# Kernel tuning notes

Measured on AMD Instinct MI355X. Metric: run time of the kernel, lower is better.

The kernel has to match this reference:

```python
import jax, jax.numpy as jnp
import numpy as np

N = 100000
E = 1250000
D = 64
K = 3
A_COEF = 1.0
B_COEF = 1.0
L_DOM = -1.0
R_DOM = 1.0


def setup_inputs() -> dict:
    key = jax.random.key(0)
    k1, k2, k3, k4, k5 = jax.random.split(key, 5)
    x = jax.random.normal(k1, (N, D), dtype=jnp.float32)
    edge_index = jax.random.randint(k2, (2, E), 0, N, dtype=jnp.int64)
    edge_weight = jax.random.uniform(k3, (E,), dtype=jnp.float32)
    alpha_params = jnp.ones((K + 1,), dtype=jnp.float32)
    lin_w = jax.random.normal(k4, ((K + 1) * D, D), dtype=jnp.float32) / np.sqrt((K + 1) * D)
    lin_b = jnp.zeros((D,), dtype=jnp.float32)
    return {"x": x, "edge_index": edge_index, "edge_weight": edge_weight,
            "alpha_params": alpha_params, "lin_w": lin_w, "lin_b": lin_b}


def reference(x, edge_index, edge_weight, alpha_params, lin_w, lin_b):
    row, col = edge_index[0], edge_index[1]
    # gcn normalization: deg from source nodes, deg<0.5 -> +1
    deg = jax.ops.segment_sum(jnp.ones((E,), x.dtype), row, num_segments=N)
    deg = jnp.where(deg < 0.5, deg + 1.0, deg)
    dis = deg ** -0.5
    val = dis[row] * edge_weight * dis[col]  # [E]

    def spmm(h):  # adj @ h : out[row] += val * h[col]
        return jax.ops.segment_sum(val[:, None] * h[col], row, num_segments=N)

    alphas = jnp.tanh(alpha_params)  # basealpha = 1.0
    a, b, l, r = A_COEF, B_COEF, L_DOM, R_DOM
    xs = [x]
    for L in range(1, K + 1):
        Ax = spmm(xs[-1])
        if L == 1:
            coef1 = (a - b) / 2 - (a + b + 2) / 2 * ((l + r) / (r - l))
            coef2 = (a + b + 2) / (r - l)
            nxt = alphas[0] * (coef1 * xs[-1] + coef2 * Ax)
        else:
            coef_l = 2 * L * (L + a + b) * (2 * L - 2 + a + b)
            coef_lm1_1 = (2 * L + a + b - 1) * (2 * L + a + b) * (2 * L + a + b - 2)
            coef_lm1_2 = (2 * L + a + b - 1) * (a ** 2 - b ** 2)
            coef_lm2 = 2 * (L - 1 + a) * (L - 1 + b) * (2 * L + a + b)
            tmp1 = alphas[L - 1] * (coef_lm1_1 / coef_l)
            tmp2 = alphas[L - 1] * (coef_lm1_2 / coef_l)
            tmp3 = alphas[L - 1] * alphas[L - 2] * (coef_lm2 / coef_l)
            tmp1_2 = tmp1 * (2.0 / (r - l))
            tmp2_2 = tmp1 * ((r + l) / (r - l)) + tmp2
            nxt = tmp1_2 * Ax - tmp2_2 * xs[-1] - tmp3 * xs[-2]
        xs.append(nxt)
    x_cat = jnp.concatenate(xs, axis=1)  # [N, (K+1)*D]
    return x_cat @ lin_w + lin_b
```

## Files before the change

### kernel.cpp

```cpp
#include <hip/hip_runtime.h>
#include <hip/hip_bf16.h>
#include <math.h>

#define NN 100000
#define EE 1250000
#define DD 64

typedef __attribute__((ext_vector_type(8))) short short8;
typedef __attribute__((ext_vector_type(4))) float f32x4;

__device__ __forceinline__ unsigned short f2b(float f) {
    unsigned u = __float_as_uint(f);
    u += 0x7fffu + ((u >> 16) & 1u);
    return (unsigned short)(u >> 16);
}
__device__ __forceinline__ float b2f(unsigned short h) {
    return __uint_as_float(((unsigned)h) << 16);
}

__global__ __launch_bounds__(256) void scan_a(const int* __restrict__ degi,
                                              int* __restrict__ rowStart,
                                              int* __restrict__ bs, int N) {
    __shared__ int s[256];
    int tid = threadIdx.x;
    int i = blockIdx.x * 256 + tid;
    int v = (i < N) ? degi[i] : 0;
    s[tid] = v;
    __syncthreads();
    for (int off = 1; off < 256; off <<= 1) {
        int t = (tid >= off) ? s[tid - off] : 0;
        __syncthreads();
        s[tid] += t;
        __syncthreads();
    }
    if (i < N) rowStart[i] = s[tid] - v;
    if (tid == 255) bs[blockIdx.x] = s[255];
}

__global__ __launch_bounds__(512) void scan_b(int* __restrict__ bs, int nb) {
    __shared__ int s[512];
    int tid = threadIdx.x;
    int v = (tid < nb) ? bs[tid] : 0;
    s[tid] = v;
    __syncthreads();
    for (int off = 1; off < 512; off <<= 1) {
        int t = (tid >= off) ? s[tid - off] : 0;
        __syncthreads();
        s[tid] += t;
        __syncthreads();
    }
    if (tid < nb) bs[tid] = s[tid] - v;
}

__global__ __launch_bounds__(256) void scan_c(int* __restrict__ rowStart,
                                              const int* __restrict__ bs,
                                              int N, int E) {
    int i = blockIdx.x * 256 + threadIdx.x;
    if (i < N) rowStart[i] += bs[blockIdx.x];
    if (i == 0) rowStart[N] = E;
}

__global__ __launch_bounds__(256) void dis_kernel(const int* __restrict__ degi,
                                                  float* __restrict__ dis, int N) {
    int i = blockIdx.x * 256 + threadIdx.x;
    if (i >= N) return;
    int d = degi[i];
    float df = (d == 0) ? 1.0f : (float)d;
    dis[i] = 1.0f / sqrtf(df);
}

#define NSL 125
#define SLR 800
#define NSEG 16
#define SEGCAP 768
#define CPAD 16
#define VSCL (1.0f / 32768.0f)
__global__ __launch_bounds__(256) void binA(const int* __restrict__ row,
                                            const int* __restrict__ col,
                                            const float* __restrict__ w,
                                            uint2* __restrict__ sbuf,
                                            int* __restrict__ segCnt, int E4) {
    __shared__ int cnt[NSL];
    __shared__ int base[NSL];
    int tid = threadIdx.x;
    if (tid < NSL) cnt[tid] = 0;
    __syncthreads();
    int g = blockIdx.x & (NSEG - 1);
    int i4 = blockIdx.x * 256 + tid;
    bool act = (i4 < E4);
    int4 r4, c4;
    float4 w4;
    int sl[4], loc[4], rk[4];
    unsigned evp[4];
    if (act) {
        r4 = ((const int4*)row)[i4];
        c4 = ((const int4*)col)[i4];
        w4 = ((const float4*)w)[i4];
        int rr[4] = {r4.x, r4.y, r4.z, r4.w};
        int cc[4] = {c4.x, c4.y, c4.z, c4.w};
        float ww[4] = {w4.x, w4.y, w4.z, w4.w};
        #pragma unroll
        for (int k = 0; k < 4; ++k) {
            int r = rr[k], c = cc[k];
            int wq = (int)(ww[k] * 32768.0f + 0.5f);
            wq = (wq > 32767) ? 32767 : wq;
            evp[k] = ((unsigned)c << 15) | (unsigned)wq;
            rk[k] = r;
            sl[k] = r / SLR;
            loc[k] = atomicAdd(&cnt[sl[k]], 1);
        }
    }
    __syncthreads();
    if (tid < NSL) {
        int c = cnt[tid];
        if (c) base[tid] = atomicAdd(&segCnt[(tid * NSEG + g) * CPAD], c);
    }
    __syncthreads();
    if (act) {
        #pragma unroll
        for (int k = 0; k < 4; ++k) {
            int p = base[sl[k]] + loc[k];
            if (p < SEGCAP)
                sbuf[(size_t)(sl[k] * NSEG + g) * SEGCAP + p] =
                    make_uint2(evp[k], (unsigned)rk[k]);
        }
    }
}

__global__ __launch_bounds__(512) void deg_slice(const uint2* __restrict__ sbuf,
                                                 const int* __restrict__ segCnt,
                                                 int* __restrict__ degi) {
    __shared__ int dcnt[SLR];
    __shared__ int scnt[NSEG];
    int tid = threadIdx.x;
    int s = blockIdx.x;
    int r0 = s * SLR;
    for (int i = tid; i < SLR; i += 512) dcnt[i] = 0;
    if (tid < NSEG) {
        int c = segCnt[(s * NSEG + tid) * CPAD];
        scnt[tid] = (c > SEGCAP) ? SEGCAP : c;
    }
    __syncthreads();
    for (int slot = tid * 4; slot < NSEG * SEGCAP; slot += 2048) {
        int g = slot / SEGCAP;
        int off = slot - g * SEGCAP;
        int cg = scnt[g];
        if (off >= cg) continue;
        const uint2* seg = sbuf + (size_t)(s * NSEG + g) * SEGCAP;
        uint4 a = *(const uint4*)(seg + off);
        uint4 b = *(const uint4*)(seg + off + 2);
        atomicAdd(&dcnt[(int)a.y - r0], 1);
        if (off + 1 < cg) atomicAdd(&dcnt[(int)a.w - r0], 1);
        if (off + 2 < cg) atomicAdd(&dcnt[(int)b.y - r0], 1);
        if (off + 3 < cg) atomicAdd(&dcnt[(int)b.w - r0], 1);
    }
    __syncthreads();
    for (int i = tid; i < SLR; i += 512) {
        int gr = r0 + i;
        if (gr < NN) degi[gr] = dcnt[i];
    }
}

__global__ __launch_bounds__(512) void binB(const uint2* __restrict__ sbuf,
                                            const int* __restrict__ segCnt,
                                            const int* __restrict__ rowStart,
                                            const float* __restrict__ dis,
                                            unsigned* __restrict__ ev) {
    __shared__ int curs[SLR];
    __shared__ int rs[SLR];
    __shared__ float dsl[SLR];
    __shared__ int scnt[NSEG];
    int tid = threadIdx.x;
    int s = blockIdx.x;
    int r0 = s * SLR;
    for (int i = tid; i < SLR; i += 512) {
        curs[i] = 0;
        int gr = r0 + i;
        rs[i] = (gr < NN) ? rowStart[gr] : 0;
        dsl[i] = (gr < NN) ? dis[gr] : 1.0f;
    }
    if (tid < NSEG) {
        int c = segCnt[(s * NSEG + tid) * CPAD];
        scnt[tid] = (c > SEGCAP) ? SEGCAP : c;
    }
    __syncthreads();
    for (int slot = tid * 4; slot < NSEG * SEGCAP; slot += 2048) {
        int g = slot / SEGCAP;
        int off = slot - g * SEGCAP;
        int cg = scnt[g];
        if (off >= cg) continue;
        const uint2* seg = sbuf + (size_t)(s * NSEG + g) * SEGCAP;
        uint4 a = *(const uint4*)(seg + off);
        uint4 b = *(const uint4*)(seg + off + 2);
        unsigned pk[4] = {a.x, a.z, b.x, b.z};
        unsigned rr[4] = {a.y, a.w, b.y, b.w};
        int nv = cg - off;
        nv = (nv > 4) ? 4 : nv;
        #pragma unroll 4
        for (int k = 0; k < 4; ++k) {
            if (k >= nv) break;
            int rl = (int)rr[k] - r0;
            int c = (int)(pk[k] >> 15);
            float wv = (float)(pk[k] & 0x7fffu) * VSCL;
            float v = dsl[rl] * wv * dis[c];
            int vq = (int)(v * 32768.0f + 0.5f);
            vq = (vq > 32767) ? 32767 : vq;
            ev[rs[rl] + atomicAdd(&curs[rl], 1)] = ((unsigned)c << 15) | (unsigned)vq;
        }
    }
}

__global__ void coef_kernel(const float* __restrict__ ap, float* __restrict__ coef) {
    if (threadIdx.x != 0 || blockIdx.x != 0) return;
    const float a = 1.0f, b = 1.0f, l = -1.0f, r = 1.0f;
    float als[3];
    als[0] = tanhf(ap[0]);
    als[1] = tanhf(ap[1]);
    als[2] = tanhf(ap[2]);
    float coef1 = (a - b) * 0.5f - (a + b + 2.0f) * 0.5f * ((l + r) / (r - l));
    float coef2 = (a + b + 2.0f) / (r - l);
    coef[0] = als[0] * coef1;
    coef[1] = als[0] * coef2;
    for (int L = 2; L <= 3; ++L) {
        float Lf = (float)L;
        float coef_l     = 2.0f * Lf * (Lf + a + b) * (2.0f * Lf - 2.0f + a + b);
        float coef_lm1_1 = (2.0f * Lf + a + b - 1.0f) * (2.0f * Lf + a + b) * (2.0f * Lf + a + b - 2.0f);
        float coef_lm1_2 = (2.0f * Lf + a + b - 1.0f) * (a * a - b * b);
        float coef_lm2   = 2.0f * (Lf - 1.0f + a) * (Lf - 1.0f + b) * (2.0f * Lf + a + b);
        float tmp1   = als[L - 1] * (coef_lm1_1 / coef_l);
        float tmp2   = als[L - 1] * (coef_lm1_2 / coef_l);
        float tmp3   = als[L - 1] * als[L - 2] * (coef_lm2 / coef_l);
        float tmp1_2 = tmp1 * (2.0f / (r - l));
        float tmp2_2 = tmp1 * ((r + l) / (r - l)) + tmp2;
        int base = 2 + (L - 2) * 3;
        coef[base + 0] = tmp1_2;
        coef[base + 1] = tmp2_2;
        coef[base + 2] = tmp3;
    }
}

__global__ __launch_bounds__(256) void tobf16(const float4* __restrict__ in,
                                              ushort4* __restrict__ outb, int n4) {
    int i = blockIdx.x * 256 + threadIdx.x;
    if (i >= n4) return;
    float4 v = in[i];
    ushort4 o;
    o.x = f2b(v.x); o.y = f2b(v.y); o.z = f2b(v.z); o.w = f2b(v.w);
    outb[i] = o;
}

__global__ __launch_bounds__(256) void wt_kernel(const float* __restrict__ W,
                                                 unsigned short* __restrict__ Wt) {
    int idx = blockIdx.x * 256 + threadIdx.x;
    int n = idx >> 8, k = idx & 255;
    Wt[idx] = f2b(W[k * 64 + n]);
}

template <int MODE>
__global__ __launch_bounds__(256) void spmm_fused(const int* __restrict__ rowStart,
                                                  const unsigned* __restrict__ ev,
                                                  const ushort4* __restrict__ hb,
                                                  const ushort4* __restrict__ xm1,
                                                  const ushort4* __restrict__ xm2,
                                                  ushort4* __restrict__ outb,
                                                  const float* __restrict__ coef,
                                                  int cbase, int N) {
    int t = blockIdx.x * 256 + threadIdx.x;
    int r = t >> 4;
    if (r >= N) return;
    int q = t & 15;
    int s0 = rowStart[r];
    int s1 = rowStart[r + 1];
    float4 acc = make_float4(0.f, 0.f, 0.f, 0.f);
    int j = s0;
    for (; j + 3 < s1; j += 4) {
        unsigned u0 = ev[j];
        unsigned u1 = ev[j + 1];
        unsigned u2 = ev[j + 2];
        unsigned u3 = ev[j + 3];
        ushort4 h0 = hb[(size_t)(u0 >> 15) * 16 + q];
        ushort4 h1 = hb[(size_t)(u1 >> 15) * 16 + q];
        ushort4 h2 = hb[(size_t)(u2 >> 15) * 16 + q];
        ushort4 h3 = hb[(size_t)(u3 >> 15) * 16 + q];
        float v0 = (float)(u0 & 0x7fffu) * VSCL;
        float v1 = (float)(u1 & 0x7fffu) * VSCL;
        float v2 = (float)(u2 & 0x7fffu) * VSCL;
        float v3 = (float)(u3 & 0x7fffu) * VSCL;
        acc.x += v0 * b2f(h0.x) + v1 * b2f(h1.x) + v2 * b2f(h2.x) + v3 * b2f(h3.x);
        acc.y += v0 * b2f(h0.y) + v1 * b2f(h1.y) + v2 * b2f(h2.y) + v3 * b2f(h3.y);
        acc.z += v0 * b2f(h0.z) + v1 * b2f(h1.z) + v2 * b2f(h2.z) + v3 * b2f(h3.z);
        acc.w += v0 * b2f(h0.w) + v1 * b2f(h1.w) + v2 * b2f(h2.w) + v3 * b2f(h3.w);
    }
    for (; j < s1; ++j) {
        unsigned u0 = ev[j];
        ushort4 h0 = hb[(size_t)(u0 >> 15) * 16 + q];
        float v0 = (float)(u0 & 0x7fffu) * VSCL;
        acc.x += v0 * b2f(h0.x);
        acc.y += v0 * b2f(h0.y);
        acc.z += v0 * b2f(h0.z);
        acc.w += v0 * b2f(h0.w);
    }
    size_t oi = (size_t)r * 16 + q;
    float4 o;
    if (MODE == 0) {
        float c0 = coef[cbase], c1 = coef[cbase + 1];
        ushort4 m1 = xm1[oi];
        o.x = c0 * b2f(m1.x) + c1 * acc.x;
        o.y = c0 * b2f(m1.y) + c1 * acc.y;
        o.z = c0 * b2f(m1.z) + c1 * acc.z;
        o.w = c0 * b2f(m1.w) + c1 * acc.w;
    } else {
        float c0 = coef[cbase], c1 = coef[cbase + 1], c2 = coef[cbase + 2];
        ushort4 m1 = xm1[oi];
        ushort4 m2 = xm2[oi];
        o.x = c0 * acc.x - c1 * b2f(m1.x) - c2 * b2f(m2.x);
        o.y = c0 * acc.y - c1 * b2f(m1.y) - c2 * b2f(m2.y);
        o.z = c0 * acc.z - c1 * b2f(m1.z) - c2 * b2f(m2.z);
        o.w = c0 * acc.w - c1 * b2f(m1.w) - c2 * b2f(m2.w);
    }
    ushort4 ob;
    ob.x = f2b(o.x); ob.y = f2b(o.y); ob.z = f2b(o.z); ob.w = f2b(o.w);
    outb[oi] = ob;
}

#define XLD 264
__global__ __launch_bounds__(256) void final_gemm_mfma(
        const ushort4* __restrict__ x0,
        const ushort4* __restrict__ x1,
        const ushort4* __restrict__ x2,
        const ushort4* __restrict__ x3,
        const unsigned short* __restrict__ Wt,
        const float* __restrict__ bias,
        float* __restrict__ out) {
    __shared__ unsigned short Xb[64 * XLD];
    const int tid = threadIdx.x;
    const int lane = tid & 63;
    const int w = tid >> 6;
    const int m = lane & 15;
    const int quad = lane >> 4;
    const int n0 = (int)blockIdx.x * 64;

    #pragma unroll 1
    for (int seg = 0; seg < 4; ++seg) {
        const ushort4* p = (seg == 0) ? x0 : (seg == 1) ? x1 : (seg == 2) ? x2 : x3;
        #pragma unroll
        for (int j = 0; j < 4; ++j) {
            int idx = tid + 256 * j;
            int r = idx >> 4, c4 = idx & 15;
            int gr = n0 + r;
            ushort4 hv = (gr < NN) ? p[(size_t)gr * 16 + c4] : make_ushort4(0, 0, 0, 0);
            *(ushort4*)&Xb[r * XLD + seg * 64 + c4 * 4] = hv;
        }
    }
    __syncthreads();

    f32x4 acc[4];
    #pragma unroll
    for (int nt = 0; nt < 4; ++nt) acc[nt] = (f32x4){0.f, 0.f, 0.f, 0.f};

    #pragma unroll 1
    for (int ks = 0; ks < 8; ++ks) {
        short8 af = *(const short8*)&Xb[(16 * w + m) * XLD + ks * 32 + quad * 8];
        #pragma unroll
        for (int nt = 0; nt < 4; ++nt) {
            short8 bf = *(const short8*)&Wt[(nt * 16 + m) * 256 + ks * 32 + quad * 8];
            acc[nt] = __builtin_amdgcn_mfma_f32_16x16x32_bf16(af, bf, acc[nt], 0, 0, 0);
        }
    }

    #pragma unroll
    for (int nt = 0; nt < 4; ++nt) {
        float bv = bias[nt * 16 + m];
        #pragma unroll
        for (int rg = 0; rg < 4; ++rg) {
            int node = n0 + 16 * w + quad * 4 + rg;
            if (node < NN) out[(size_t)node * 64 + nt * 16 + m] = acc[nt][rg] + bv;
        }
    }
}

extern "C" void kernel_launch(void* const* d_in, const int* in_sizes, int n_in,
                              void* d_out, int out_size, void* d_ws, size_t ws_size,
                              hipStream_t stream) {
    const float* x  = (const float*)d_in[0];
    const int*   ei = (const int*)d_in[1];
    const float* ew = (const float*)d_in[2];
    const float* ap = (const float*)d_in[3];
    const float* lw = (const float*)d_in[4];
    const float* lb = (const float*)d_in[5];
    float* out = (float*)d_out;

    const int N = NN, E = EE;
    const int ND = N * DD;

    const int* row = ei;
    const int* col = ei + E;

    char* ws = (char*)d_ws;
    ushort4* xb = (ushort4*)ws;
    ushort4* Ab = (ushort4*)(ws + (size_t)ND * 2);
    ushort4* Bb = (ushort4*)(ws + (size_t)ND * 4);
    ushort4* Cb = (ushort4*)(ws + (size_t)ND * 6);
    uint2*   sbuf   = (uint2*)(ws + (size_t)ND * 4);
    int*     segCnt = (int*)(ws + (size_t)ND * 6);
    unsigned* ev = (unsigned*)(ws + (size_t)ND * 8);
    char* sm    = ws + (size_t)ND * 8 + (size_t)E * 4;
    float* coef     = (float*)sm;
    float* dis      = (float*)(sm + 256);
    int*   degi     = (int*)(sm + 256 + (size_t)N * 4);
    int*   rowStart = (int*)(sm + 256 + (size_t)N * 8);
    int*   bs       = (int*)(sm + 256 + (size_t)N * 12 + 64);
    unsigned short* Wt = (unsigned short*)(sm + 256 + (size_t)N * 12 + 64 + 4096);

    const int gridN  = (N + 255) / 256;
    const int gridSp = (N * 16) / 256;
    const int gridCv = (ND / 4) / 256;
    const int gridG  = (N + 63) / 64;
    const int E4     = E / 4;
    const int gridA  = (E4 + 255) / 256;

    hipMemsetAsync(segCnt, 0, (size_t)NSL * NSEG * CPAD * 4, stream);
    coef_kernel<<<1, 64, 0, stream>>>(ap, coef);
    wt_kernel<<<64, 256, 0, stream>>>(lw, Wt);
    binA<<<gridA, 256, 0, stream>>>(row, col, ew, sbuf, segCnt, E4);
    deg_slice<<<NSL, 512, 0, stream>>>(sbuf, segCnt, degi);
    scan_a<<<gridN, 256, 0, stream>>>(degi, rowStart, bs, N);
    scan_b<<<1, 512, 0, stream>>>(bs, gridN);
    scan_c<<<gridN, 256, 0, stream>>>(rowStart, bs, N, E);
    dis_kernel<<<gridN, 256, 0, stream>>>(degi, dis, N);
    binB<<<NSL, 512, 0, stream>>>(sbuf, segCnt, rowStart, dis, ev);

    tobf16<<<gridCv, 256, 0, stream>>>((const float4*)x, xb, ND / 4);

    spmm_fused<0><<<gridSp, 256, 0, stream>>>(rowStart, ev, xb, xb, xb,
                                              Ab, coef, 0, N);
    spmm_fused<1><<<gridSp, 256, 0, stream>>>(rowStart, ev, Ab, Ab, xb,
                                              Bb, coef, 2, N);
    spmm_fused<1><<<gridSp, 256, 0, stream>>>(rowStart, ev, Bb, Bb, Ab,
                                              Cb, coef, 5, N);

    final_gemm_mfma<<<gridG, 256, 0, stream>>>(xb, Ab, Bb, Cb, Wt, lb, out);
}
```

Baseline: 279.5 us.

## Load GEMM A-fragments directly from global and process 128 rows per block

The final projection GEMM no longer stages the concatenated bf16 features through shared memory. Each wave now loads its MFMA A-fragments straight from global memory and computes two 16-row tiles, so each block covers 128 nodes and every Wt fragment load is reused twice. The aim is to drop the LDS staging, its barrier and its shared-memory footprint, and to halve weight reloads per node, at the cost of more accumulator registers and uncoalesced 16-byte global reads.

```diff
diff --git a/kernel.cpp b/kernel.cpp
--- a/kernel.cpp
+++ b/kernel.cpp
@@ -323,8 +323,7 @@
     outb[oi] = ob;
 }
 
-#define XLD 264
-__global__ __launch_bounds__(256) void final_gemm_mfma(
+__global__ __launch_bounds__(256, 4) void final_gemm_mfma(
         const ushort4* __restrict__ x0,
         const ushort4* __restrict__ x1,
         const ushort4* __restrict__ x2,
@@ -332,39 +331,36 @@
         const unsigned short* __restrict__ Wt,
         const float* __restrict__ bias,
         float* __restrict__ out) {
-    __shared__ unsigned short Xb[64 * XLD];
     const int tid = threadIdx.x;
     const int lane = tid & 63;
     const int w = tid >> 6;
     const int m = lane & 15;
     const int quad = lane >> 4;
-    const int n0 = (int)blockIdx.x * 64;
-
-    #pragma unroll 1
-    for (int seg = 0; seg < 4; ++seg) {
-        const ushort4* p = (seg == 0) ? x0 : (seg == 1) ? x1 : (seg == 2) ? x2 : x3;
-        #pragma unroll
-        for (int j = 0; j < 4; ++j) {
-            int idx = tid + 256 * j;
-            int r = idx >> 4, c4 = idx & 15;
-            int gr = n0 + r;
-            ushort4 hv = (gr < NN) ? p[(size_t)gr * 16 + c4] : make_ushort4(0, 0, 0, 0);
-            *(ushort4*)&Xb[r * XLD + seg * 64 + c4 * 4] = hv;
-        }
-    }
-    __syncthreads();
-
-    f32x4 acc[4];
+    const int n0 = (int)blockIdx.x * 128;
+
+    int gr0 = n0 + 16 * w + m;
+    int gr1 = gr0 + 64;
+    size_t ar0 = (size_t)((gr0 < NN) ? gr0 : 0) * 16;
+    size_t ar1 = (size_t)((gr1 < NN) ? gr1 : 0) * 16;
+
+    f32x4 acc0[4], acc1[4];
     #pragma unroll
-    for (int nt = 0; nt < 4; ++nt) acc[nt] = (f32x4){0.f, 0.f, 0.f, 0.f};
-
-    #pragma unroll 1
+    for (int nt = 0; nt < 4; ++nt) {
+        acc0[nt] = (f32x4){0.f, 0.f, 0.f, 0.f};
+        acc1[nt] = (f32x4){0.f, 0.f, 0.f, 0.f};
+    }
+
+    #pragma unroll
     for (int ks = 0; ks < 8; ++ks) {
-        short8 af = *(const short8*)&Xb[(16 * w + m) * XLD + ks * 32 + quad * 8];
+        const ushort4* p = (ks < 2) ? x0 : (ks < 4) ? x1 : (ks < 6) ? x2 : x3;
+        size_t ko = (size_t)((ks & 1) * 8 + quad * 2);
+        short8 af0 = *(const short8*)&p[ar0 + ko];
+        short8 af1 = *(const short8*)&p[ar1 + ko];
         #pragma unroll
         for (int nt = 0; nt < 4; ++nt) {
             short8 bf = *(const short8*)&Wt[(nt * 16 + m) * 256 + ks * 32 + quad * 8];
-            acc[nt] = __builtin_amdgcn_mfma_f32_16x16x32_bf16(af, bf, acc[nt], 0, 0, 0);
+            acc0[nt] = __builtin_amdgcn_mfma_f32_16x16x32_bf16(af0, bf, acc0[nt], 0, 0, 0);
+            acc1[nt] = __builtin_amdgcn_mfma_f32_16x16x32_bf16(af1, bf, acc1[nt], 0, 0, 0);
         }
     }
 
@@ -373,8 +369,10 @@
         float bv = bias[nt * 16 + m];
         #pragma unroll
         for (int rg = 0; rg < 4; ++rg) {
-            int node = n0 + 16 * w + quad * 4 + rg;
-            if (node < NN) out[(size_t)node * 64 + nt * 16 + m] = acc[nt][rg] + bv;
+            int node0 = n0 + 16 * w + quad * 4 + rg;
+            int node1 = node0 + 64;
+            if (node0 < NN) out[(size_t)node0 * 64 + nt * 16 + m] = acc0[nt][rg] + bv;
+            if (node1 < NN) out[(size_t)node1 * 64 + nt * 16 + m] = acc1[nt][rg] + bv;
         }
     }
 }
@@ -415,7 +413,7 @@
     const int gridN  = (N + 255) / 256;
     const int gridSp = (N * 16) / 256;
     const int gridCv = (ND / 4) / 256;
-    const int gridG  = (N + 63) / 64;
+    const int gridG  = (N + 127) / 128;
     const int E4     = E / 4;
     const int gridA  = (E4 + 255) / 256;
 
```

Result: faster. 262.4 us (-6.1%).
